# Kernel tuning notes

Hardware: AMD Instinct MI355X
Metric: run time of the kernel (lower is better)

The kernel has to match this reference:

```python
import jax, jax.numpy as jnp
import numpy as np

B, H, Q, K, D = 2, 8, 512, 512, 64


def setup_inputs() -> dict:
    key = jax.random.key(0)
    ks = jax.random.split(key, 8)
    s = 1.0 / np.sqrt(D)
    return {
        "query": jax.random.normal(ks[0], (B, H, Q, D), dtype=jnp.float32),
        "keys": jax.random.normal(ks[1], (B, H, K, D), dtype=jnp.float32),
        "Wa_w": jax.random.normal(ks[2], (D, D), dtype=jnp.float32) * s,
        "Wa_b": jax.random.normal(ks[3], (D,), dtype=jnp.float32) * s,
        "Ua_w": jax.random.normal(ks[4], (D, D), dtype=jnp.float32) * s,
        "Ua_b": jax.random.normal(ks[5], (D,), dtype=jnp.float32) * s,
        "V_w": jax.random.normal(ks[6], (D,), dtype=jnp.float32) * s,
        "V_b": jax.random.normal(ks[7], (1,), dtype=jnp.float32) * s,
    }


def reference(query, keys, Wa_w, Wa_b, Ua_w, Ua_b, V_w, V_b):
    # Linear projections (torch Linear: x @ W.T + b)
    q_proj = jnp.einsum("bhqd,ed->bhqe", query, Wa_w) + Wa_b  # [B,H,Q,D]
    k_proj = jnp.einsum("bhkd,ed->bhke", keys, Ua_w) + Ua_b   # [B,H,K,D]
    # Broadcast add + tanh -> [B,H,Q,K,D] (the fusion-headroom intermediate)
    features = jnp.tanh(q_proj[:, :, :, None, :] + k_proj[:, :, None, :, :])
    # Linear reduce D -> scalar, squeeze last dim
    scores = jnp.einsum("bhqkd,d->bhqk", features, V_w) + V_b[0]  # [B,H,Q,K]
    return scores
```

## Files before the change

kernel.cpp:

```cpp
#include <hip/hip_runtime.h>


#define BHX 16
#define SEQ 512
#define DDIM 64

__global__ __launch_bounds__(256) void proj_kernel(
    const float* __restrict__ query, const float* __restrict__ keys,
    const float* __restrict__ Wa_w,  const float* __restrict__ Wa_b,
    const float* __restrict__ Ua_w,  const float* __restrict__ Ua_b,
    float* __restrict__ eq, float* __restrict__ hk)
{
  const int t = threadIdx.x, lane = t & 63, wave = t >> 6;
  const bool is_k = blockIdx.x >= 512;
  const float* __restrict__ X  = is_k ? keys : query;
  const float* __restrict__ W  = is_k ? Ua_w : Wa_w;
  const float* __restrict__ Bv = is_k ? Ua_b : Wa_b;
  float* __restrict__ out      = is_k ? hk : eq;
  const int row0 = (blockIdx.x & 511) * 16;

  float w[64];
  const float4* W4 = (const float4*)(W + lane * DDIM);
#pragma unroll
  for (int i = 0; i < 16; ++i) {
    float4 v = W4[i];
    w[4*i] = v.x; w[4*i+1] = v.y; w[4*i+2] = v.z; w[4*i+3] = v.w;
  }
#pragma unroll
  for (int i = 0; i < 16; ++i)
    asm volatile("" : "+v"(w[4*i]), "+v"(w[4*i+1]), "+v"(w[4*i+2]), "+v"(w[4*i+3]));

  const float C = 2.885390081777926815f;
  const float b = Bv[lane];
  const float sgn = is_k ? -C : C;

#pragma unroll 1
  for (int i = 0; i < 4; ++i) {
    const int r   = row0 + wave * 4 + i;
    const int off = __builtin_amdgcn_readfirstlane(r * DDIM);
    const float* xr = X + off;
    float a0 = 0, a1 = 0, a2 = 0, a3 = 0;
#pragma unroll
    for (int e = 0; e < 64; e += 4) {
      a0 = __builtin_fmaf(xr[e],     w[e],     a0);
      a1 = __builtin_fmaf(xr[e + 1], w[e + 1], a1);
      a2 = __builtin_fmaf(xr[e + 2], w[e + 2], a2);
      a3 = __builtin_fmaf(xr[e + 3], w[e + 3], a3);
    }
    float p = ((a0 + a1) + (a2 + a3)) + b;
    out[(size_t)r * DDIM + lane] = __builtin_amdgcn_exp2f(sgn * p);
  }
}

__global__ __launch_bounds__(256) void score_kernel(
    const float* __restrict__ eq,
    const float* __restrict__ hk,
    const float* __restrict__ Vw,
    const float* __restrict__ Vb,
    float* __restrict__ out)
{
  __shared__ float hk_l[64][65];
  __shared__ float vh_l[64][65];

  const int bh   = blockIdx.z;
  const int q0   = blockIdx.y * 64;
  const int k0   = blockIdx.x * 64;
  const int lane = threadIdx.x & 63;
  const int wave = threadIdx.x >> 6;

  const float vwl = Vw[lane];
  {
    const float* base = hk + (size_t)(bh * SEQ + k0 + wave * 16) * DDIM;
#pragma unroll
    for (int r = 0; r < 16; ++r) {
      float h = base[r * DDIM + lane];
      hk_l[lane][wave * 16 + r] = h;
      vh_l[lane][wave * 16 + r] = vwl * h;
    }
  }

  float acc0 = Vb[0];
#pragma unroll
  for (int d = 0; d < 64; ++d) acc0 += Vw[d];

  __syncthreads();

#pragma unroll 1
  for (int jp = 0; jp < 4; ++jp) {
    const int q    = q0 + wave * 16 + jp * 4;
    const int off  = __builtin_amdgcn_readfirstlane((bh * SEQ + q) * DDIM);
    const float* qr0 = eq + off;
    const float* qr1 = qr0 + DDIM;
    const float* qr2 = qr1 + DDIM;
    const float* qr3 = qr2 + DDIM;
    float ac0 = 0.f, ac1 = 0.f, ac2 = 0.f, ac3 = 0.f;
#pragma unroll 1
    for (int c = 0; c < 4; ++c) {
#pragma unroll
      for (int p = 0; p < 8; ++p) {
        const int d = c * 16 + p * 2;
        const float h0 = hk_l[d][lane],     h1 = hk_l[d + 1][lane];
        const float v0 = vh_l[d][lane],     v1 = vh_l[d + 1][lane];
        {
          float A = h0 + qr0[d], B = h1 + qr0[d + 1];
          float num = __builtin_fmaf(v1, A, v0 * B);
          ac0 = __builtin_fmaf(num, __builtin_amdgcn_rcpf(A * B), ac0);
        }
        {
          float A = h0 + qr1[d], B = h1 + qr1[d + 1];
          float num = __builtin_fmaf(v1, A, v0 * B);
          ac1 = __builtin_fmaf(num, __builtin_amdgcn_rcpf(A * B), ac1);
        }
        {
          float A = h0 + qr2[d], B = h1 + qr2[d + 1];
          float num = __builtin_fmaf(v1, A, v0 * B);
          ac2 = __builtin_fmaf(num, __builtin_amdgcn_rcpf(A * B), ac2);
        }
        {
          float A = h0 + qr3[d], B = h1 + qr3[d + 1];
          float num = __builtin_fmaf(v1, A, v0 * B);
          ac3 = __builtin_fmaf(num, __builtin_amdgcn_rcpf(A * B), ac3);
        }
      }
    }
    const size_t ob = (size_t)(bh * SEQ + q) * SEQ + k0 + lane;
    out[ob]           = __builtin_fmaf(-2.f, ac0, acc0);
    out[ob + SEQ]     = __builtin_fmaf(-2.f, ac1, acc0);
    out[ob + 2 * SEQ] = __builtin_fmaf(-2.f, ac2, acc0);
    out[ob + 3 * SEQ] = __builtin_fmaf(-2.f, ac3, acc0);
  }
}

extern "C" void kernel_launch(void* const* d_in, const int* in_sizes, int n_in,
                              void* d_out, int out_size, void* d_ws, size_t ws_size,
                              hipStream_t stream) {
  const float* query = (const float*)d_in[0];
  const float* keys  = (const float*)d_in[1];
  const float* Wa_w  = (const float*)d_in[2];
  const float* Wa_b  = (const float*)d_in[3];
  const float* Ua_w  = (const float*)d_in[4];
  const float* Ua_b  = (const float*)d_in[5];
  const float* V_w   = (const float*)d_in[6];
  const float* V_b   = (const float*)d_in[7];
  float* out = (float*)d_out;

  const int R = BHX * SEQ;
  float* eq = (float*)d_ws;
  float* hk = eq + (size_t)R * DDIM;

  proj_kernel<<<1024, 256, 0, stream>>>(query, keys, Wa_w, Wa_b,
                                        Ua_w, Ua_b, eq, hk);

  dim3 grid(SEQ / 64, SEQ / 64, BHX);
  score_kernel<<<grid, 256, 0, stream>>>(eq, hk, V_w, V_b, out);
}
```

Baseline: 48.70 us.

## Hoist key features into registers per chunk and halve query tile

The score kernel now loads 16 key-feature values per D-chunk into registers once, then reuses them across 8 query rows instead of re-reading LDS for each group of 4 queries. The separate V-weighted LDS array is removed and recomputed in registers from Vw, which lowers LDS footprint. The query tile shrinks from 64 to 32 rows per block, doubling the grid. The added register pressure may reduce occupancy, and the per-query accumulator now depends on sequential FMAs with less ILP.

Result: slower. 57.40 us (+17.9%).

```diff
diff --git a/kernel.cpp b/kernel.cpp
--- a/kernel.cpp
+++ b/kernel.cpp
@@ -4,6 +4,8 @@
 #define BHX 16
 #define SEQ 512
 #define DDIM 64
+#define QT 32
+#define KT 64
 
 __global__ __launch_bounds__(256) void proj_kernel(
     const float* __restrict__ query, const float* __restrict__ keys,
@@ -60,23 +62,18 @@
     float* __restrict__ out)
 {
   __shared__ float hk_l[64][65];
-  __shared__ float vh_l[64][65];
 
   const int bh   = blockIdx.z;
-  const int q0   = blockIdx.y * 64;
-  const int k0   = blockIdx.x * 64;
+  const int q0   = blockIdx.y * QT;
+  const int k0   = blockIdx.x * KT;
   const int lane = threadIdx.x & 63;
   const int wave = threadIdx.x >> 6;
 
-  const float vwl = Vw[lane];
   {
     const float* base = hk + (size_t)(bh * SEQ + k0 + wave * 16) * DDIM;
 #pragma unroll
-    for (int r = 0; r < 16; ++r) {
-      float h = base[r * DDIM + lane];
-      hk_l[lane][wave * 16 + r] = h;
-      vh_l[lane][wave * 16 + r] = vwl * h;
-    }
+    for (int r = 0; r < 16; ++r)
+      hk_l[lane][wave * 16 + r] = base[r * DDIM + lane];
   }
 
   float acc0 = Vb[0];
@@ -85,49 +82,46 @@
 
   __syncthreads();
 
+  float acc[8] = {0.f, 0.f, 0.f, 0.f, 0.f, 0.f, 0.f, 0.f};
+  const int qbase =
+      __builtin_amdgcn_readfirstlane((bh * SEQ + q0 + wave * 8) * DDIM);
+
 #pragma unroll 1
-  for (int jp = 0; jp < 4; ++jp) {
-    const int q    = q0 + wave * 16 + jp * 4;
-    const int off  = __builtin_amdgcn_readfirstlane((bh * SEQ + q) * DDIM);
-    const float* qr0 = eq + off;
-    const float* qr1 = qr0 + DDIM;
-    const float* qr2 = qr1 + DDIM;
-    const float* qr3 = qr2 + DDIM;
-    float ac0 = 0.f, ac1 = 0.f, ac2 = 0.f, ac3 = 0.f;
-#pragma unroll 1
-    for (int c = 0; c < 4; ++c) {
+  for (int c = 0; c < 4; ++c) {
+    float h[16], vh[16];
+#pragma unroll
+    for (int j = 0; j < 16; ++j) h[j] = hk_l[c * 16 + j][lane];
+#pragma unroll
+    for (int j = 0; j < 16; ++j) vh[j] = Vw[c * 16 + j] * h[j];
+    asm volatile("" : "+v"(h[0]), "+v"(h[1]), "+v"(h[2]), "+v"(h[3]),
+                      "+v"(h[4]), "+v"(h[5]), "+v"(h[6]), "+v"(h[7]));
+    asm volatile("" : "+v"(h[8]),  "+v"(h[9]),  "+v"(h[10]), "+v"(h[11]),
+                      "+v"(h[12]), "+v"(h[13]), "+v"(h[14]), "+v"(h[15]));
+    asm volatile("" : "+v"(vh[0]), "+v"(vh[1]), "+v"(vh[2]), "+v"(vh[3]),
+                      "+v"(vh[4]), "+v"(vh[5]), "+v"(vh[6]), "+v"(vh[7]));
+    asm volatile("" : "+v"(vh[8]),  "+v"(vh[9]),  "+v"(vh[10]), "+v"(vh[11]),
+                      "+v"(vh[12]), "+v"(vh[13]), "+v"(vh[14]), "+v"(vh[15]));
+
+#pragma unroll 2
+    for (int qi = 0; qi < 8; ++qi) {
+      const float* qr = eq + qbase + qi * DDIM + c * 16;
+      float a = 0.f;
 #pragma unroll
       for (int p = 0; p < 8; ++p) {
-        const int d = c * 16 + p * 2;
-        const float h0 = hk_l[d][lane],     h1 = hk_l[d + 1][lane];
-        const float v0 = vh_l[d][lane],     v1 = vh_l[d + 1][lane];
-        {
-          float A = h0 + qr0[d], B = h1 + qr0[d + 1];
-          float num = __builtin_fmaf(v1, A, v0 * B);
-          ac0 = __builtin_fmaf(num, __builtin_amdgcn_rcpf(A * B), ac0);
-        }
-        {
-          float A = h0 + qr1[d], B = h1 + qr1[d + 1];
-          float num = __builtin_fmaf(v1, A, v0 * B);
-          ac1 = __builtin_fmaf(num, __builtin_amdgcn_rcpf(A * B), ac1);
-        }
-        {
-          float A = h0 + qr2[d], B = h1 + qr2[d + 1];
-          float num = __builtin_fmaf(v1, A, v0 * B);
-          ac2 = __builtin_fmaf(num, __builtin_amdgcn_rcpf(A * B), ac2);
-        }
-        {
-          float A = h0 + qr3[d], B = h1 + qr3[d + 1];
-          float num = __builtin_fmaf(v1, A, v0 * B);
-          ac3 = __builtin_fmaf(num, __builtin_amdgcn_rcpf(A * B), ac3);
-        }
+        const float A = h[2*p]     + qr[2*p];
+        const float B = h[2*p + 1] + qr[2*p + 1];
+        const float num = __builtin_fmaf(vh[2*p + 1], A, vh[2*p] * B);
+        a = __builtin_fmaf(num, __builtin_amdgcn_rcpf(A * B), a);
       }
+      acc[qi] += a;
     }
-    const size_t ob = (size_t)(bh * SEQ + q) * SEQ + k0 + lane;
-    out[ob]           = __builtin_fmaf(-2.f, ac0, acc0);
-    out[ob + SEQ]     = __builtin_fmaf(-2.f, ac1, acc0);
-    out[ob + 2 * SEQ] = __builtin_fmaf(-2.f, ac2, acc0);
-    out[ob + 3 * SEQ] = __builtin_fmaf(-2.f, ac3, acc0);
+  }
+
+#pragma unroll
+  for (int qi = 0; qi < 8; ++qi) {
+    const size_t ob =
+        (size_t)(bh * SEQ + q0 + wave * 8 + qi) * SEQ + k0 + lane;
+    out[ob] = __builtin_fmaf(-2.f, acc[qi], acc0);
   }
 }
 
@@ -151,6 +145,6 @@
   proj_kernel<<<1024, 256, 0, stream>>>(query, keys, Wa_w, Wa_b,
                                         Ua_w, Ua_b, eq, hk);
 
-  dim3 grid(SEQ / 64, SEQ / 64, BHX);
+  dim3 grid(SEQ / KT, SEQ / QT, BHX);
   score_kernel<<<grid, 256, 0, stream>>>(eq, hk, V_w, V_b, out);
 }
```
